# Kernel tuning notes

Hardware: AMD Instinct MI355X
Metric: run time of the kernel (lower is better)

Reference implementation:

```python
import jax, jax.numpy as jnp
import numpy as np

D_MODEL, D_K, D_V = 1024, 64, 64
B, S = 4, 2048

def setup_inputs() -> dict:
    key = jax.random.key(0)
    ks = jax.random.split(key, 9)
    lim = 1.0 / np.sqrt(D_MODEL)
    return {
        "query": jax.random.normal(ks[0], (B, S, D_MODEL), jnp.float32),
        "key":   jax.random.normal(ks[1], (B, S, D_MODEL), jnp.float32),
        "value": jax.random.normal(ks[2], (B, S, D_MODEL), jnp.float32),
        "Wq": jax.random.uniform(ks[3], (D_MODEL, D_K), jnp.float32, -lim, lim),
        "bq": jax.random.uniform(ks[4], (D_K,), jnp.float32, -lim, lim),
        "Wk": jax.random.uniform(ks[5], (D_MODEL, D_K), jnp.float32, -lim, lim),
        "bk": jax.random.uniform(ks[6], (D_K,), jnp.float32, -lim, lim),
        "Wv": jax.random.uniform(ks[7], (D_MODEL, D_V), jnp.float32, -lim, lim),
        "bv": jax.random.uniform(ks[8], (D_V,), jnp.float32, -lim, lim),
    }

def reference(query, key, value, Wq, bq, Wk, bk, Wv, bv):
    # Linear projections: [B,S,d_model] -> [B,S,d_k/d_v]
    q = jnp.einsum("bsd,dk->bsk", query, Wq) + bq
    k = jnp.einsum("bsd,dk->bsk", key, Wk) + bk
    v = jnp.einsum("bsd,dv->bsv", value, Wv) + bv
    scale = 1.0 / jnp.sqrt(jnp.asarray(q.shape[-1], q.dtype))
    scores = jnp.einsum("bqk,bsk->bqs", q, k) * scale  # [B,S,S]
    attn = jax.nn.softmax(scores, axis=-1)
    return jnp.einsum("bqs,bsv->bqv", attn, v)  # [B,S,d_v]
```

## Files before the change

kernel.cpp:

```cpp
#include <hip/hip_runtime.h>
#include <hip/hip_bf16.h>


typedef __attribute__((ext_vector_type(8))) short bf16x8;
typedef __attribute__((ext_vector_type(4))) float f32x4;

#define MFMA16(a, b, c) __builtin_amdgcn_mfma_f32_16x16x32_bf16((a), (b), (c), 0, 0, 0)

__device__ __forceinline__ unsigned short f2bf(float x) {
    unsigned int u = __float_as_uint(x);
    u = (u + 0x7FFFu + ((u >> 16) & 1u)) >> 16;
    return (unsigned short)u;
}

__global__ __launch_bounds__(256) void prep_w(
    const float* __restrict__ Wq, const float* __restrict__ Wk,
    const float* __restrict__ Wv, unsigned short* __restrict__ Wt) {
    int idx = blockIdx.x * 256 + threadIdx.x;
    int t = idx >> 16;
    int r = idx & 0xFFFF;
    int n = r >> 10, kk = r & 1023;
    const float* W = (t == 0) ? Wq : ((t == 1) ? Wk : Wv);
    Wt[idx] = f2bf(W[kk * 64 + n]);
}

__global__ __launch_bounds__(256) void proj_kernel(
    const float* __restrict__ xq, const float* __restrict__ xk,
    const float* __restrict__ xv, const unsigned short* __restrict__ Wt,
    const float* __restrict__ bq, const float* __restrict__ bk,
    const float* __restrict__ bv, unsigned short* __restrict__ outq,
    unsigned short* __restrict__ outk, unsigned short* __restrict__ outvt) {
    const int chunk = blockIdx.x;
    const int t = chunk >> 8;
    const int rb = chunk & 255;
    const int row0 = rb * 32;
    const float* __restrict__ x = (t == 0) ? xq : ((t == 1) ? xk : xv);
    const float* __restrict__ bias = (t == 0) ? bq : ((t == 1) ? bk : bv);
    const unsigned short* __restrict__ Wtt = Wt + t * 65536;

    __shared__ __align__(16) unsigned short xl[2][32][72];
    __shared__ __align__(16) unsigned short wl[2][64][72];

    const int tid = threadIdx.x;
    const int w = tid >> 6, l = tid & 63;
    const int lo = l & 15, q4 = l >> 4;
    const int rowt = (w & 1) * 16;
    const int colb = (w >> 1) * 32;

    const int lr = tid >> 3;
    const int lkc = (tid & 7) * 8;
    const int wr = tid >> 2;
    const int wkc = (tid & 3) * 16;

    f32x4 acc[2];
    for (int i = 0; i < 2; i++)
        for (int j = 0; j < 4; j++) acc[i][j] = 0.f;

    const float* xrow = x + (size_t)(row0 + lr) * 1024 + lkc;
    const unsigned short* wrow = Wtt + (size_t)wr * 1024 + wkc;

    float4 pxA0, pxA1, pxB0, pxB1;
    int4 pwA0, pwA1, pwB0, pwB1;

#define LOADSET(X0, X1, W0, W1, s)                                            \
    do {                                                                      \
        const float* xn = xrow + (s) * 64;                                    \
        X0 = *(const float4*)(xn);                                            \
        X1 = *(const float4*)(xn + 4);                                        \
        const unsigned short* wn = wrow + (s) * 64;                           \
        W0 = *(const int4*)(wn);                                              \
        W1 = *(const int4*)(wn + 8);                                          \
    } while (0)

#define WRITESET(X0, X1, W0, W1, bi)                                          \
    do {                                                                      \
        int4 d;                                                               \
        d.x = f2bf(X0.x) | ((int)f2bf(X0.y) << 16);                           \
        d.y = f2bf(X0.z) | ((int)f2bf(X0.w) << 16);                           \
        d.z = f2bf(X1.x) | ((int)f2bf(X1.y) << 16);                           \
        d.w = f2bf(X1.z) | ((int)f2bf(X1.w) << 16);                           \
        *(int4*)&xl[bi][lr][lkc] = d;                                         \
        *(int4*)&wl[bi][wr][wkc] = W0;                                        \
        *(int4*)&wl[bi][wr][wkc + 8] = W1;                                    \
    } while (0)

#define COMPUTE(bi)                                                           \
    do {                                                                      \
        bf16x8 a0 = *(const bf16x8*)&xl[bi][rowt + lo][q4 * 8];               \
        bf16x8 a1 = *(const bf16x8*)&xl[bi][rowt + lo][32 + q4 * 8];          \
        _Pragma("unroll")                                                     \
        for (int ci = 0; ci < 2; ++ci) {                                      \
            bf16x8 b0 = *(const bf16x8*)&wl[bi][colb + ci * 16 + lo][q4 * 8]; \
            bf16x8 b1 =                                                       \
                *(const bf16x8*)&wl[bi][colb + ci * 16 + lo][32 + q4 * 8];    \
            acc[ci] = MFMA16(a0, b0, acc[ci]);                                \
            acc[ci] = MFMA16(a1, b1, acc[ci]);                                \
        }                                                                     \
    } while (0)

    LOADSET(pxA0, pxA1, pwA0, pwA1, 0);
    WRITESET(pxA0, pxA1, pwA0, pwA1, 0);
    LOADSET(pxB0, pxB1, pwB0, pwB1, 1);
    LOADSET(pxA0, pxA1, pwA0, pwA1, 2);
    __syncthreads();

#pragma unroll
    for (int ss = 0; ss < 8; ++ss) {
        const int s = ss * 2;
        if (s < 15) WRITESET(pxB0, pxB1, pwB0, pwB1, 1);
        if (s < 13) LOADSET(pxB0, pxB1, pwB0, pwB1, s + 3);
        COMPUTE(0);
        __syncthreads();
        if (s + 1 < 15) WRITESET(pxA0, pxA1, pwA0, pwA1, 0);
        if (s + 1 < 13) LOADSET(pxA0, pxA1, pwA0, pwA1, s + 4);
        COMPUTE(1);
        __syncthreads();
    }
#undef LOADSET
#undef WRITESET
#undef COMPUTE

#pragma unroll
    for (int ci = 0; ci < 2; ++ci) {
        float bb = bias[colb + ci * 16 + lo];
#pragma unroll
        for (int i = 0; i < 4; i++) acc[ci][i] += bb;
    }
    if (t == 0) {
        const float SC = 0.125f * 1.44269504088896340736f;
#pragma unroll
        for (int ci = 0; ci < 2; ++ci)
#pragma unroll
            for (int i = 0; i < 4; i++) acc[ci][i] *= SC;
    }
    if (t < 2) {
        unsigned short* out = (t == 0) ? outq : outk;
#pragma unroll
        for (int ci = 0; ci < 2; ++ci)
#pragma unroll
            for (int i = 0; i < 4; i++)
                out[(size_t)(row0 + rowt + q4 * 4 + i) * 64 + colb + ci * 16 + lo] =
                    f2bf(acc[ci][i]);
    } else {
        int b = row0 >> 11;
        int sl = (row0 & 2047) + rowt + q4 * 4;
#pragma unroll
        for (int ci = 0; ci < 2; ++ci) {
            int vf = colb + ci * 16 + lo;
            ushort4 h;
            h.x = f2bf(acc[ci][0]);
            h.y = f2bf(acc[ci][1]);
            h.z = f2bf(acc[ci][2]);
            h.w = f2bf(acc[ci][3]);
            *(ushort4*)&outvt[(size_t)(b * 64 + vf) * 2048 + sl] = h;
        }
    }
}

__global__ __launch_bounds__(512) void flash_kernel(
    const unsigned short* __restrict__ q, const unsigned short* __restrict__ k,
    const unsigned short* __restrict__ vt, float* __restrict__ out) {
    const int bx = blockIdx.x;
    const int xcd = bx & 7;
    const int b = xcd >> 1;
    const int qb = ((bx >> 3) << 1) | (xcd & 1);
    const int w = threadIdx.x >> 6, l = threadIdx.x & 63;
    const int lo = l & 15, q4 = l >> 4;

    __shared__ __align__(16) unsigned short pl[8][16][72];
    __shared__ __align__(16) float Olds[8][16][64];
    __shared__ float lds_l[8][16];

    const int srow = qb * 16;

    const unsigned short* qp = q + (size_t)(b * 2048 + srow + lo) * 64 + q4 * 8;
    bf16x8 aq0 = *(const bf16x8*)(qp);
    bf16x8 aq1 = *(const bf16x8*)(qp + 32);

    f32x4 O[4];
    for (int i = 0; i < 4; i++)
        for (int j2 = 0; j2 < 4; j2++) O[i][j2] = 0.f;
    float ll[4] = {0.f, 0.f, 0.f, 0.f};

    for (int kt = 0; kt < 4; ++kt) {
        const int kb = w * 256 + kt * 64;
        f32x4 S[4];
        for (int i = 0; i < 4; i++)
            for (int j2 = 0; j2 < 4; j2++) S[i][j2] = 0.f;
        const unsigned short* kp = k + (size_t)(b * 2048 + kb + lo) * 64 + q4 * 8;
#pragma unroll
        for (int ct = 0; ct < 4; ++ct) {
            bf16x8 b0 = *(const bf16x8*)(kp + ct * 1024);
            bf16x8 b1 = *(const bf16x8*)(kp + ct * 1024 + 32);
            S[ct] = MFMA16(aq0, b0, S[ct]);
            S[ct] = MFMA16(aq1, b1, S[ct]);
        }
#pragma unroll
        for (int i = 0; i < 4; i++) {
#pragma unroll
            for (int ct = 0; ct < 4; ++ct) {
                float p = exp2f(S[ct][i]);
                S[ct][i] = p;
                ll[i] += p;
            }
#pragma unroll
            for (int ct = 0; ct < 4; ++ct)
                pl[w][q4 * 4 + i][ct * 16 + lo] = f2bf(S[ct][i]);
        }
        bf16x8 ap0 = *(const bf16x8*)&pl[w][lo][q4 * 8];
        bf16x8 ap1 = *(const bf16x8*)&pl[w][lo][32 + q4 * 8];
        const unsigned short* vp =
            vt + (size_t)(b * 64 + lo) * 2048 + kb + q4 * 8;
#pragma unroll
        for (int ct = 0; ct < 4; ++ct) {
            bf16x8 v0 = *(const bf16x8*)(vp + (size_t)ct * 16 * 2048);
            bf16x8 v1 = *(const bf16x8*)(vp + (size_t)ct * 16 * 2048 + 32);
            O[ct] = MFMA16(ap0, v0, O[ct]);
            O[ct] = MFMA16(ap1, v1, O[ct]);
        }
    }

#pragma unroll
    for (int ct = 0; ct < 4; ++ct)
#pragma unroll
        for (int i = 0; i < 4; i++)
            Olds[w][q4 * 4 + i][ct * 16 + lo] = O[ct][i];
#pragma unroll
    for (int i = 0; i < 4; i++) {
        float s = ll[i];
        s += __shfl_xor(s, 1);
        s += __shfl_xor(s, 2);
        s += __shfl_xor(s, 4);
        s += __shfl_xor(s, 8);
        if (lo == 0) lds_l[w][q4 * 4 + i] = s;
    }
    __syncthreads();

    const int row = threadIdx.x >> 5;
    const int cp = threadIdx.x & 31;
    float L = 0.f;
#pragma unroll
    for (int ww = 0; ww < 8; ++ww) L += lds_l[ww][row];
    const float inv = 1.f / L;
    float sx = 0.f, sy = 0.f;
#pragma unroll
    for (int ww = 0; ww < 8; ++ww) {
        const float2 o = *(const float2*)&Olds[ww][row][cp * 2];
        sx += o.x;
        sy += o.y;
    }
    float2 r = make_float2(sx * inv, sy * inv);
    *(float2*)&out[((size_t)(b * 2048 + srow + row)) * 64 + cp * 2] = r;
}

extern "C" void kernel_launch(void* const* d_in, const int* in_sizes, int n_in,
                              void* d_out, int out_size, void* d_ws,
                              size_t ws_size, hipStream_t stream) {
    const float* xq = (const float*)d_in[0];
    const float* xk = (const float*)d_in[1];
    const float* xv = (const float*)d_in[2];
    const float* Wq = (const float*)d_in[3];
    const float* bq = (const float*)d_in[4];
    const float* Wk = (const float*)d_in[5];
    const float* bk = (const float*)d_in[6];
    const float* Wv = (const float*)d_in[7];
    const float* bv = (const float*)d_in[8];
    float* out = (float*)d_out;

    char* ws = (char*)d_ws;
    unsigned short* qb = (unsigned short*)(ws);
    unsigned short* kb = (unsigned short*)(ws + (1u << 20));
    unsigned short* vtb = (unsigned short*)(ws + (2u << 20));
    unsigned short* Wt = (unsigned short*)(ws + (3u << 20));

    hipLaunchKernelGGL(prep_w, dim3(768), dim3(256), 0, stream, Wq, Wk, Wv, Wt);
    hipLaunchKernelGGL(proj_kernel, dim3(768), dim3(256), 0, stream, xq, xk, xv,
                       Wt, bq, bk, bv, qb, kb, vtb);
    hipLaunchKernelGGL(flash_kernel, dim3(512), dim3(512), 0, stream, qb, kb,
                       vtb, out);
}
```

Before: 171.5 us.

## Fuse projection and attention into one persistent launch with per-batch atomic counters

Merges the projection and flash-attention kernels into a single launch. The first 384 blocks each run two projection sub-tiles and increment a per-batch counter. The remaining 512 blocks spin on that counter until their batch's Q/K/V are complete, then compute attention. This removes one kernel launch boundary and lets attention for early batches overlap with projection of later ones. The risks are spin-wait stalls, deadlock if waiting blocks occupy the CUs before the producers are scheduled, and the cost of the larger shared-memory footprint and 512-thread projection blocks.

Result: slower. 268.4 us (+56.5%).

```diff
diff --git a/kernel.cpp b/kernel.cpp
--- a/kernel.cpp
+++ b/kernel.cpp
@@ -15,8 +15,10 @@
 
 __global__ __launch_bounds__(256) void prep_w(
     const float* __restrict__ Wq, const float* __restrict__ Wk,
-    const float* __restrict__ Wv, unsigned short* __restrict__ Wt) {
+    const float* __restrict__ Wv, unsigned short* __restrict__ Wt,
+    unsigned int* __restrict__ cnt) {
     int idx = blockIdx.x * 256 + threadIdx.x;
+    if (idx < 4) cnt[idx] = 0u;
     int t = idx >> 16;
     int r = idx & 0xFFFF;
     int n = r >> 10, kk = r & 1023;
@@ -24,43 +26,52 @@
     Wt[idx] = f2bf(W[kk * 64 + n]);
 }
 
-__global__ __launch_bounds__(256) void proj_kernel(
+__global__ __launch_bounds__(512) void fused_kernel(
     const float* __restrict__ xq, const float* __restrict__ xk,
     const float* __restrict__ xv, const unsigned short* __restrict__ Wt,
     const float* __restrict__ bq, const float* __restrict__ bk,
     const float* __restrict__ bv, unsigned short* __restrict__ outq,
-    unsigned short* __restrict__ outk, unsigned short* __restrict__ outvt) {
-    const int chunk = blockIdx.x;
-    const int t = chunk >> 8;
-    const int rb = chunk & 255;
-    const int row0 = rb * 32;
-    const float* __restrict__ x = (t == 0) ? xq : ((t == 1) ? xk : xv);
-    const float* __restrict__ bias = (t == 0) ? bq : ((t == 1) ? bk : bv);
-    const unsigned short* __restrict__ Wtt = Wt + t * 65536;
-
-    __shared__ __align__(16) unsigned short xl[2][32][72];
-    __shared__ __align__(16) unsigned short wl[2][64][72];
-
-    const int tid = threadIdx.x;
-    const int w = tid >> 6, l = tid & 63;
-    const int lo = l & 15, q4 = l >> 4;
-    const int rowt = (w & 1) * 16;
-    const int colb = (w >> 1) * 32;
-
-    const int lr = tid >> 3;
-    const int lkc = (tid & 7) * 8;
-    const int wr = tid >> 2;
-    const int wkc = (tid & 3) * 16;
-
-    f32x4 acc[2];
-    for (int i = 0; i < 2; i++)
-        for (int j = 0; j < 4; j++) acc[i][j] = 0.f;
-
-    const float* xrow = x + (size_t)(row0 + lr) * 1024 + lkc;
-    const unsigned short* wrow = Wtt + (size_t)wr * 1024 + wkc;
-
-    float4 pxA0, pxA1, pxB0, pxB1;
-    int4 pwA0, pwA1, pwB0, pwB1;
+    unsigned short* __restrict__ outk, unsigned short* __restrict__ outvt,
+    float* __restrict__ out, unsigned int* __restrict__ cnt) {
+    __shared__ __align__(16) char smem[55296];
+
+    if (blockIdx.x < 384) {
+        const int sub = threadIdx.x >> 8;
+        const int tid = threadIdx.x & 255;
+        const int c = blockIdx.x * 2 + sub;
+        const int bat = c / 192;
+        const int r = c % 192;
+        const int t = r >> 6;
+        const int rb = bat * 64 + (r & 63);
+        const int row0 = rb * 32;
+        const float* __restrict__ x = (t == 0) ? xq : ((t == 1) ? xk : xv);
+        const float* __restrict__ bias = (t == 0) ? bq : ((t == 1) ? bk : bv);
+        const unsigned short* __restrict__ Wtt = Wt + t * 65536;
+
+        unsigned short(*xl)[32][72] =
+            (unsigned short(*)[32][72])(smem + sub * 27648);
+        unsigned short(*wl)[64][72] =
+            (unsigned short(*)[64][72])(smem + sub * 27648 + 9216);
+
+        const int w = tid >> 6, l = tid & 63;
+        const int lo = l & 15, q4 = l >> 4;
+        const int rowt = (w & 1) * 16;
+        const int colb = (w >> 1) * 32;
+
+        const int lr = tid >> 3;
+        const int lkc = (tid & 7) * 8;
+        const int wr = tid >> 2;
+        const int wkc = (tid & 3) * 16;
+
+        f32x4 acc[2];
+        for (int i = 0; i < 2; i++)
+            for (int j = 0; j < 4; j++) acc[i][j] = 0.f;
+
+        const float* xrow = x + (size_t)(row0 + lr) * 1024 + lkc;
+        const unsigned short* wrow = Wtt + (size_t)wr * 1024 + wkc;
+
+        float4 pxA0, pxA1, pxB0, pxB1;
+        int4 pwA0, pwA1, pwB0, pwB1;
 
 #define LOADSET(X0, X1, W0, W1, s)                                            \
     do {                                                                      \
@@ -98,159 +109,173 @@
         }                                                                     \
     } while (0)
 
-    LOADSET(pxA0, pxA1, pwA0, pwA1, 0);
-    WRITESET(pxA0, pxA1, pwA0, pwA1, 0);
-    LOADSET(pxB0, pxB1, pwB0, pwB1, 1);
-    LOADSET(pxA0, pxA1, pwA0, pwA1, 2);
-    __syncthreads();
-
-#pragma unroll
-    for (int ss = 0; ss < 8; ++ss) {
-        const int s = ss * 2;
-        if (s < 15) WRITESET(pxB0, pxB1, pwB0, pwB1, 1);
-        if (s < 13) LOADSET(pxB0, pxB1, pwB0, pwB1, s + 3);
-        COMPUTE(0);
+        LOADSET(pxA0, pxA1, pwA0, pwA1, 0);
+        WRITESET(pxA0, pxA1, pwA0, pwA1, 0);
+        LOADSET(pxB0, pxB1, pwB0, pwB1, 1);
+        LOADSET(pxA0, pxA1, pwA0, pwA1, 2);
         __syncthreads();
-        if (s + 1 < 15) WRITESET(pxA0, pxA1, pwA0, pwA1, 0);
-        if (s + 1 < 13) LOADSET(pxA0, pxA1, pwA0, pwA1, s + 4);
-        COMPUTE(1);
-        __syncthreads();
-    }
+
+#pragma unroll
+        for (int ss = 0; ss < 8; ++ss) {
+            const int s = ss * 2;
+            if (s < 15) WRITESET(pxB0, pxB1, pwB0, pwB1, 1);
+            if (s < 13) LOADSET(pxB0, pxB1, pwB0, pwB1, s + 3);
+            COMPUTE(0);
+            __syncthreads();
+            if (s + 1 < 15) WRITESET(pxA0, pxA1, pwA0, pwA1, 0);
+            if (s + 1 < 13) LOADSET(pxA0, pxA1, pwA0, pwA1, s + 4);
+            COMPUTE(1);
+            __syncthreads();
+        }
 #undef LOADSET
 #undef WRITESET
 #undef COMPUTE
 
 #pragma unroll
-    for (int ci = 0; ci < 2; ++ci) {
-        float bb = bias[colb + ci * 16 + lo];
-#pragma unroll
-        for (int i = 0; i < 4; i++) acc[ci][i] += bb;
+        for (int ci = 0; ci < 2; ++ci) {
+            float bb = bias[colb + ci * 16 + lo];
+#pragma unroll
+            for (int i = 0; i < 4; i++) acc[ci][i] += bb;
+        }
+        if (t == 0) {
+            const float SC = 0.125f * 1.44269504088896340736f;
+#pragma unroll
+            for (int ci = 0; ci < 2; ++ci)
+#pragma unroll
+                for (int i = 0; i < 4; i++) acc[ci][i] *= SC;
+        }
+        if (t < 2) {
+            unsigned short* o = (t == 0) ? outq : outk;
+#pragma unroll
+            for (int ci = 0; ci < 2; ++ci)
+#pragma unroll
+                for (int i = 0; i < 4; i++)
+                    o[(size_t)(row0 + rowt + q4 * 4 + i) * 64 + colb + ci * 16 +
+                      lo] = f2bf(acc[ci][i]);
+        } else {
+            int b = row0 >> 11;
+            int sl = (row0 & 2047) + rowt + q4 * 4;
+#pragma unroll
+            for (int ci = 0; ci < 2; ++ci) {
+                int vf = colb + ci * 16 + lo;
+                ushort4 h;
+                h.x = f2bf(acc[ci][0]);
+                h.y = f2bf(acc[ci][1]);
+                h.z = f2bf(acc[ci][2]);
+                h.w = f2bf(acc[ci][3]);
+                *(ushort4*)&outvt[(size_t)(b * 64 + vf) * 2048 + sl] = h;
+            }
+        }
+        __syncthreads();
+        if (tid == 0)
+            __hip_atomic_fetch_add(&cnt[bat], 1u, __ATOMIC_RELEASE,
+                                   __HIP_MEMORY_SCOPE_AGENT);
+    } else {
+        const int fid = blockIdx.x - 384;
+        const int xcd = fid & 7;
+        const int b = xcd >> 1;
+        const int qb = ((fid >> 3) << 1) | (xcd & 1);
+
+        if (threadIdx.x == 0) {
+            while (__hip_atomic_load(&cnt[b], __ATOMIC_ACQUIRE,
+                                     __HIP_MEMORY_SCOPE_AGENT) < 192u)
+                __builtin_amdgcn_s_sleep(32);
+        }
+        __syncthreads();
+
+        unsigned short(*pl)[16][72] = (unsigned short(*)[16][72])smem;
+        float(*Olds)[16][64] = (float(*)[16][64])(smem + 18432);
+        float(*lds_l)[16] = (float(*)[16])(smem + 51200);
+
+        const unsigned short* q = outq;
+        const unsigned short* k = outk;
+        const unsigned short* vt = outvt;
+
+        const int w = threadIdx.x >> 6, l = threadIdx.x & 63;
+        const int lo = l & 15, q4 = l >> 4;
+        const int srow = qb * 16;
+
+        const unsigned short* qp =
+            q + (size_t)(b * 2048 + srow + lo) * 64 + q4 * 8;
+        bf16x8 aq0 = *(const bf16x8*)(qp);
+        bf16x8 aq1 = *(const bf16x8*)(qp + 32);
+
+        f32x4 O[4];
+        for (int i = 0; i < 4; i++)
+            for (int j2 = 0; j2 < 4; j2++) O[i][j2] = 0.f;
+        float ll[4] = {0.f, 0.f, 0.f, 0.f};
+
+        for (int kt = 0; kt < 4; ++kt) {
+            const int kb = w * 256 + kt * 64;
+            f32x4 S[4];
+            for (int i = 0; i < 4; i++)
+                for (int j2 = 0; j2 < 4; j2++) S[i][j2] = 0.f;
+            const unsigned short* kp =
+                k + (size_t)(b * 2048 + kb + lo) * 64 + q4 * 8;
+#pragma unroll
+            for (int ct = 0; ct < 4; ++ct) {
+                bf16x8 b0 = *(const bf16x8*)(kp + ct * 1024);
+                bf16x8 b1 = *(const bf16x8*)(kp + ct * 1024 + 32);
+                S[ct] = MFMA16(aq0, b0, S[ct]);
+                S[ct] = MFMA16(aq1, b1, S[ct]);
+            }
+#pragma unroll
+            for (int i = 0; i < 4; i++) {
+#pragma unroll
+                for (int ct = 0; ct < 4; ++ct) {
+                    float p = exp2f(S[ct][i]);
+                    S[ct][i] = p;
+                    ll[i] += p;
+                }
+#pragma unroll
+                for (int ct = 0; ct < 4; ++ct)
+                    pl[w][q4 * 4 + i][ct * 16 + lo] = f2bf(S[ct][i]);
+            }
+            bf16x8 ap0 = *(const bf16x8*)&pl[w][lo][q4 * 8];
+            bf16x8 ap1 = *(const bf16x8*)&pl[w][lo][32 + q4 * 8];
+            const unsigned short* vp =
+                vt + (size_t)(b * 64 + lo) * 2048 + kb + q4 * 8;
+#pragma unroll
+            for (int ct = 0; ct < 4; ++ct) {
+                bf16x8 v0 = *(const bf16x8*)(vp + (size_t)ct * 16 * 2048);
+                bf16x8 v1 = *(const bf16x8*)(vp + (size_t)ct * 16 * 2048 + 32);
+                O[ct] = MFMA16(ap0, v0, O[ct]);
+                O[ct] = MFMA16(ap1, v1, O[ct]);
+            }
+        }
+
+#pragma unroll
+        for (int ct = 0; ct < 4; ++ct)
+#pragma unroll
+            for (int i = 0; i < 4; i++)
+                Olds[w][q4 * 4 + i][ct * 16 + lo] = O[ct][i];
+#pragma unroll
+        for (int i = 0; i < 4; i++) {
+            float s = ll[i];
+            s += __shfl_xor(s, 1);
+            s += __shfl_xor(s, 2);
+            s += __shfl_xor(s, 4);
+            s += __shfl_xor(s, 8);
+            if (lo == 0) lds_l[w][q4 * 4 + i] = s;
+        }
+        __syncthreads();
+
+        const int row = threadIdx.x >> 5;
+        const int cp = threadIdx.x & 31;
+        float L = 0.f;
+#pragma unroll
+        for (int ww = 0; ww < 8; ++ww) L += lds_l[ww][row];
+        const float inv = 1.f / L;
+        float sx = 0.f, sy = 0.f;
+#pragma unroll
+        for (int ww = 0; ww < 8; ++ww) {
+            const float2 o = *(const float2*)&Olds[ww][row][cp * 2];
+            sx += o.x;
+            sy += o.y;
+        }
+        float2 rr = make_float2(sx * inv, sy * inv);
+        *(float2*)&out[((size_t)(b * 2048 + srow + row)) * 64 + cp * 2] = rr;
     }
-    if (t == 0) {
-        const float SC = 0.125f * 1.44269504088896340736f;
-#pragma unroll
-        for (int ci = 0; ci < 2; ++ci)
-#pragma unroll
-            for (int i = 0; i < 4; i++) acc[ci][i] *= SC;
-    }
-    if (t < 2) {
-        unsigned short* out = (t == 0) ? outq : outk;
-#pragma unroll
-        for (int ci = 0; ci < 2; ++ci)
-#pragma unroll
-            for (int i = 0; i < 4; i++)
-                out[(size_t)(row0 + rowt + q4 * 4 + i) * 64 + colb + ci * 16 + lo] =
-                    f2bf(acc[ci][i]);
-    } else {
-        int b = row0 >> 11;
-        int sl = (row0 & 2047) + rowt + q4 * 4;
-#pragma unroll
-        for (int ci = 0; ci < 2; ++ci) {
-            int vf = colb + ci * 16 + lo;
-            ushort4 h;
-            h.x = f2bf(acc[ci][0]);
-            h.y = f2bf(acc[ci][1]);
-            h.z = f2bf(acc[ci][2]);
-            h.w = f2bf(acc[ci][3]);
-            *(ushort4*)&outvt[(size_t)(b * 64 + vf) * 2048 + sl] = h;
-        }
-    }
-}
-
-__global__ __launch_bounds__(512) void flash_kernel(
-    const unsigned short* __restrict__ q, const unsigned short* __restrict__ k,
-    const unsigned short* __restrict__ vt, float* __restrict__ out) {
-    const int bx = blockIdx.x;
-    const int xcd = bx & 7;
-    const int b = xcd >> 1;
-    const int qb = ((bx >> 3) << 1) | (xcd & 1);
-    const int w = threadIdx.x >> 6, l = threadIdx.x & 63;
-    const int lo = l & 15, q4 = l >> 4;
-
-    __shared__ __align__(16) unsigned short pl[8][16][72];
-    __shared__ __align__(16) float Olds[8][16][64];
-    __shared__ float lds_l[8][16];
-
-    const int srow = qb * 16;
-
-    const unsigned short* qp = q + (size_t)(b * 2048 + srow + lo) * 64 + q4 * 8;
-    bf16x8 aq0 = *(const bf16x8*)(qp);
-    bf16x8 aq1 = *(const bf16x8*)(qp + 32);
-
-    f32x4 O[4];
-    for (int i = 0; i < 4; i++)
-        for (int j2 = 0; j2 < 4; j2++) O[i][j2] = 0.f;
-    float ll[4] = {0.f, 0.f, 0.f, 0.f};
-
-    for (int kt = 0; kt < 4; ++kt) {
-        const int kb = w * 256 + kt * 64;
-        f32x4 S[4];
-        for (int i = 0; i < 4; i++)
-            for (int j2 = 0; j2 < 4; j2++) S[i][j2] = 0.f;
-        const unsigned short* kp = k + (size_t)(b * 2048 + kb + lo) * 64 + q4 * 8;
-#pragma unroll
-        for (int ct = 0; ct < 4; ++ct) {
-            bf16x8 b0 = *(const bf16x8*)(kp + ct * 1024);
-            bf16x8 b1 = *(const bf16x8*)(kp + ct * 1024 + 32);
-            S[ct] = MFMA16(aq0, b0, S[ct]);
-            S[ct] = MFMA16(aq1, b1, S[ct]);
-        }
-#pragma unroll
-        for (int i = 0; i < 4; i++) {
-#pragma unroll
-            for (int ct = 0; ct < 4; ++ct) {
-                float p = exp2f(S[ct][i]);
-                S[ct][i] = p;
-                ll[i] += p;
-            }
-#pragma unroll
-            for (int ct = 0; ct < 4; ++ct)
-                pl[w][q4 * 4 + i][ct * 16 + lo] = f2bf(S[ct][i]);
-        }
-        bf16x8 ap0 = *(const bf16x8*)&pl[w][lo][q4 * 8];
-        bf16x8 ap1 = *(const bf16x8*)&pl[w][lo][32 + q4 * 8];
-        const unsigned short* vp =
-            vt + (size_t)(b * 64 + lo) * 2048 + kb + q4 * 8;
-#pragma unroll
-        for (int ct = 0; ct < 4; ++ct) {
-            bf16x8 v0 = *(const bf16x8*)(vp + (size_t)ct * 16 * 2048);
-            bf16x8 v1 = *(const bf16x8*)(vp + (size_t)ct * 16 * 2048 + 32);
-            O[ct] = MFMA16(ap0, v0, O[ct]);
-            O[ct] = MFMA16(ap1, v1, O[ct]);
-        }
-    }
-
-#pragma unroll
-    for (int ct = 0; ct < 4; ++ct)
-#pragma unroll
-        for (int i = 0; i < 4; i++)
-            Olds[w][q4 * 4 + i][ct * 16 + lo] = O[ct][i];
-#pragma unroll
-    for (int i = 0; i < 4; i++) {
-        float s = ll[i];
-        s += __shfl_xor(s, 1);
-        s += __shfl_xor(s, 2);
-        s += __shfl_xor(s, 4);
-        s += __shfl_xor(s, 8);
-        if (lo == 0) lds_l[w][q4 * 4 + i] = s;
-    }
-    __syncthreads();
-
-    const int row = threadIdx.x >> 5;
-    const int cp = threadIdx.x & 31;
-    float L = 0.f;
-#pragma unroll
-    for (int ww = 0; ww < 8; ++ww) L += lds_l[ww][row];
-    const float inv = 1.f / L;
-    float sx = 0.f, sy = 0.f;
-#pragma unroll
-    for (int ww = 0; ww < 8; ++ww) {
-        const float2 o = *(const float2*)&Olds[ww][row][cp * 2];
-        sx += o.x;
-        sy += o.y;
-    }
-    float2 r = make_float2(sx * inv, sy * inv);
-    *(float2*)&out[((size_t)(b * 2048 + srow + row)) * 64 + cp * 2] = r;
 }
 
 extern "C" void kernel_launch(void* const* d_in, const int* in_sizes, int n_in,
@@ -272,10 +297,10 @@
     unsigned short* kb = (unsigned short*)(ws + (1u << 20));
     unsigned short* vtb = (unsigned short*)(ws + (2u << 20));
     unsigned short* Wt = (unsigned short*)(ws + (3u << 20));
-
-    hipLaunchKernelGGL(prep_w, dim3(768), dim3(256), 0, stream, Wq, Wk, Wv, Wt);
-    hipLaunchKernelGGL(proj_kernel, dim3(768), dim3(256), 0, stream, xq, xk, xv,
-                       Wt, bq, bk, bv, qb, kb, vtb);
-    hipLaunchKernelGGL(flash_kernel, dim3(512), dim3(512), 0, stream, qb, kb,
-                       vtb, out);
+    unsigned int* cnt = (unsigned int*)(ws + (4u << 20));
+
+    hipLaunchKernelGGL(prep_w, dim3(768), dim3(256), 0, stream, Wq, Wk, Wv, Wt,
+                       cnt);
+    hipLaunchKernelGGL(fused_kernel, dim3(896), dim3(512), 0, stream, xq, xk,
+                       xv, Wt, bq, bk, bv, qb, kb, vtb, out, cnt);
 }
```
